# Kernel tuning notes

Measured on AMD Instinct MI355X. Metric: run time of the kernel, lower is better.

Reference implementation:

```python
import jax, jax.numpy as jnp
import numpy as np


def setup_inputs() -> dict:
    key = jax.random.key(0)
    ks = jax.random.split(key, 12)
    B, T, S, H, I = 32, 32, 400, 1024, 1024
    s = 0.02  # weight init scale
    return {
        "input_": jax.random.normal(ks[0], (B, T, I), jnp.float32),
        "h0": jax.random.normal(ks[1], (B, H), jnp.float32),
        "c0": jax.random.normal(ks[2], (B, H), jnp.float32),
        "h_attn0": jax.random.normal(ks[3], (B, H), jnp.float32),
        "encoder_hy": jax.random.normal(ks[4], (S, B, H), jnp.float32),
        "past_attn": jax.random.uniform(ks[5], (B, S), jnp.float32),
        "W_ih": jax.random.normal(ks[6], (4 * H, I + H), jnp.float32) * s,
        "W_hh": jax.random.normal(ks[7], (4 * H, H), jnp.float32) * s,
        "b_ih": jnp.zeros((4 * H,), jnp.float32),
        "b_hh": jnp.zeros((4 * H,), jnp.float32),
        "W_attn": jax.random.normal(ks[8], (H, H), jnp.float32) * s,
        "W_out": jax.random.normal(ks[9], (H, 2 * H), jnp.float32) * s,
    }


def _decode(input_, h0, c0, h_attn0, encoder_hy, W_ih, W_hh, b_ih, b_hh, W_attn, W_out):
    # encoder_hy: [S, B, H] -> enhy: [B, S, H]
    enhy = jnp.transpose(encoder_hy, (1, 0, 2))
    # attn_in(enhy) is time-invariant (linear, fixed enhy): hoist out of the loop
    enhy_new = jnp.einsum("bsh,gh->bsg", enhy, W_attn)  # [B, S, H]
    xs = jnp.transpose(input_, (1, 0, 2))  # [T, B, I] (batch_first)

    def step(carry, x_k):
        h, c, h_attn = carry
        x = jnp.concatenate([x_k, h_attn], axis=1)  # [B, I+H]
        gates = x @ W_ih.T + b_ih + h @ W_hh.T + b_hh  # [B, 4H]
        i, f, g, o = jnp.split(gates, 4, axis=1)  # torch LSTMCell gate order
        i = jax.nn.sigmoid(i)
        f = jax.nn.sigmoid(f)
        g = jnp.tanh(g)
        o = jax.nn.sigmoid(o)
        c = f * c + i * g
        h = o * jnp.tanh(c)
        # luong_general: attn = bmm(attn_in(enhy), dehy)
        attn = jax.nn.softmax(jnp.einsum("bsh,bh->bs", enhy_new, h), axis=1)
        ctx = jnp.einsum("bs,bsh->bh", attn, enhy)
        h_attn = jnp.tanh(jnp.concatenate([ctx, h], axis=1) @ W_out.T)
        return (h, c, h_attn), (h_attn, attn)

    (h, c, h_attn), (outs, attns) = jax.lax.scan(step, (h0, c0, h_attn0), xs)
    output = jnp.transpose(outs, (1, 0, 2))  # [B, T, H] (batch_first)
    return output, h, c, h_attn, attns  # attns: [T, B, S]


def reference(input_, h0, c0, h_attn0, encoder_hy, past_attn,
              W_ih, W_hh, b_ih, b_hh, W_attn, W_out):
    output, h, c, h_attn, out_attn = _decode(
        input_, h0, c0, h_attn0, encoder_hy, W_ih, W_hh, b_ih, b_hh, W_attn, W_out)
    # coverage='none': past_attn passes through unchanged; loss_cv stays 0.0
    return output, h, c, h_attn, out_attn, past_attn, jnp.float32(0.0)
```

## Files before the change

kernel.cpp:

```cpp
#include <hip/hip_runtime.h>
#include <hip/hip_bf16.h>

using u16 = unsigned short;
typedef __attribute__((ext_vector_type(8))) short bf16x8;
typedef __attribute__((ext_vector_type(4))) float f32x4;
typedef __attribute__((ext_vector_type(4))) u16 u16x4;


__device__ __forceinline__ float bf2f(u16 u){ union{unsigned int i; float f;} v; v.i = ((unsigned int)u)<<16; return v.f; }
__device__ __forceinline__ u16 f2bf(float f){ __hip_bfloat16 h = __float2bfloat16(f); return *reinterpret_cast<u16*>(&h); }
struct HL { u16 h, l; };
__device__ __forceinline__ HL split1(float f){
  HL r; r.h = f2bf(f); r.l = f2bf(f - bf2f(r.h)); return r;
}
__device__ __forceinline__ f32x4 mfma16(bf16x8 a, bf16x8 b, f32x4 c){ return __builtin_amdgcn_mfma_f32_16x16x32_bf16(a,b,c,0,0,0); }


__global__ __launch_bounds__(256) void cast_wih_k(const float* __restrict__ Wih,
    u16* __restrict__ Wxh, u16* __restrict__ Wxl, u16* __restrict__ Wrh, u16* __restrict__ Wrl){
  int v = blockIdx.x*256 + threadIdx.x;
  if (v >= (4096*2048)/4) return;
  int flat = v*4; int j = flat >> 11; int k = flat & 2047;
  float4 f = *(const float4*)(Wih + flat);
  HL s0 = split1(f.x), s1 = split1(f.y), s2 = split1(f.z), s3 = split1(f.w);
  u16x4 h, l;
  h[0]=s0.h; h[1]=s1.h; h[2]=s2.h; h[3]=s3.h;
  l[0]=s0.l; l[1]=s1.l; l[2]=s2.l; l[3]=s3.l;
  if (k < 1024){
    *(u16x4*)(Wxh + (size_t)j*1024 + k) = h;
    *(u16x4*)(Wxl + (size_t)j*1024 + k) = l;
  } else {
    *(u16x4*)(Wrh + (size_t)j*2048 + (k-1024)) = h;
    *(u16x4*)(Wrl + (size_t)j*2048 + (k-1024)) = l;
  }
}

__global__ __launch_bounds__(256) void cast_whh_k(const float* __restrict__ Whh,
    u16* __restrict__ Wrh, u16* __restrict__ Wrl){
  int v = blockIdx.x*256 + threadIdx.x;
  if (v >= (4096*1024)/4) return;
  int flat = v*4; int j = flat >> 10; int k = flat & 1023;
  float4 f = *(const float4*)(Whh + flat);
  HL s0 = split1(f.x), s1 = split1(f.y), s2 = split1(f.z), s3 = split1(f.w);
  u16x4 h, l;
  h[0]=s0.h; h[1]=s1.h; h[2]=s2.h; h[3]=s3.h;
  l[0]=s0.l; l[1]=s1.l; l[2]=s2.l; l[3]=s3.l;
  *(u16x4*)(Wrh + (size_t)j*2048 + 1024 + k) = h;
  *(u16x4*)(Wrl + (size_t)j*2048 + 1024 + k) = l;
}

__global__ __launch_bounds__(256) void cast_split_k(const float* __restrict__ src,
    u16* __restrict__ dh, u16* __restrict__ dl, int n4){
  int v = blockIdx.x*256 + threadIdx.x;
  if (v >= n4) return;
  float4 f = *(const float4*)(src + (size_t)v*4);
  HL s0 = split1(f.x), s1 = split1(f.y), s2 = split1(f.z), s3 = split1(f.w);
  u16x4 h, l;
  h[0]=s0.h; h[1]=s1.h; h[2]=s2.h; h[3]=s3.h;
  l[0]=s0.l; l[1]=s1.l; l[2]=s2.l; l[3]=s3.l;
  *(u16x4*)(dh + (size_t)v*4) = h;
  *(u16x4*)(dl + (size_t)v*4) = l;
}

__global__ __launch_bounds__(256) void cast_x_k(const float* __restrict__ inp,
    u16* __restrict__ Xh, u16* __restrict__ Xl){
  int v = blockIdx.x*256 + threadIdx.x;
  if (v >= (1024*1024)/4) return;
  int flat = v*4; int m = flat >> 10; int k = flat & 1023;
  int t = m >> 5, b = m & 31;
  float4 f = *(const float4*)(inp + ((size_t)(b*32 + t) << 10) + k);
  HL s0 = split1(f.x), s1 = split1(f.y), s2 = split1(f.z), s3 = split1(f.w);
  u16x4 h, l;
  h[0]=s0.h; h[1]=s1.h; h[2]=s2.h; h[3]=s3.h;
  l[0]=s0.l; l[1]=s1.l; l[2]=s2.l; l[3]=s3.l;
  *(u16x4*)(Xh + flat) = h;
  *(u16x4*)(Xl + flat) = l;
}

__global__ __launch_bounds__(256) void watsplit_k(const float* __restrict__ Wattn,
    u16* __restrict__ Wth, u16* __restrict__ Wtl){
  __shared__ float t[32][33];
  int gx = blockIdx.x, cx = blockIdx.y;
  int ty = threadIdx.x >> 5, tx = threadIdx.x & 31;
  #pragma unroll
  for (int i=0;i<4;++i){
    int g = gx*32 + ty + i*8;
    t[ty+i*8][tx] = Wattn[(size_t)g*1024 + cx*32 + tx];
  }
  __syncthreads();
  #pragma unroll
  for (int i=0;i<4;++i){
    int c = cx*32 + ty + i*8;
    HL s = split1(t[tx][ty+i*8]);
    Wth[(size_t)c*1024 + gx*32 + tx] = s.h;
    Wtl[(size_t)c*1024 + gx*32 + tx] = s.l;
  }
}

__global__ __launch_bounds__(256) void cast_encb_k(const float* __restrict__ enc,
    u16* __restrict__ encb){
  int v = blockIdx.x*256 + threadIdx.x;
  if (v >= (400*32*1024)/8) return;
  size_t flat = (size_t)v*8;
  int c = flat & 1023; int rem = flat >> 10;
  int b = rem & 31, s = rem >> 5;
  float4 f0 = *(const float4*)(enc + flat);
  float4 f1 = *(const float4*)(enc + flat + 4);
  u16x4 h0, h1;
  h0[0]=f2bf(f0.x); h0[1]=f2bf(f0.y); h0[2]=f2bf(f0.z); h0[3]=f2bf(f0.w);
  h1[0]=f2bf(f1.x); h1[1]=f2bf(f1.y); h1[2]=f2bf(f1.z); h1[3]=f2bf(f1.w);
  u16* dst = encb + ((size_t)b*400 + s)*1024 + c;
  *(u16x4*)dst = h0;
  *(u16x4*)(dst+4) = h1;
}

__global__ __launch_bounds__(256) void init_misc_k(const float* __restrict__ h0, const float* __restrict__ c0,
    const float* __restrict__ ha0, const float* __restrict__ past,
    u16* __restrict__ Zh0, u16* __restrict__ Zl0, float* __restrict__ cbuf,
    float* __restrict__ out_past, float* __restrict__ out_loss){
  int idx = blockIdx.x*256 + threadIdx.x;
  if (idx < 65536){
    int b = idx >> 11, col = idx & 2047;
    float v = (col < 1024) ? ha0[b*1024 + col] : h0[b*1024 + col - 1024];
    HL s = split1(v);
    Zh0[idx] = s.h; Zl0[idx] = s.l;
  } else if (idx < 65536 + 32768){
    int i = idx - 65536; cbuf[i] = c0[i];
  } else if (idx < 65536 + 32768 + 12800){
    int i = idx - 98304; out_past[i] = past[i];
  } else if (idx == 65536 + 32768 + 12800){
    out_loss[0] = 0.f;
  }
}

__global__ __launch_bounds__(256) void gemm128_bias_k(
    const u16* __restrict__ Ah, const u16* __restrict__ Al,
    const u16* __restrict__ Bh, const u16* __restrict__ Bl, float* __restrict__ C,
    const float* __restrict__ bias0, const float* __restrict__ bias1, int M, int N, int K)
{
  __shared__ __align__(16) u16 Ash[4096], Asl[4096], Bsh[4096], Bsl[4096];
  const int tid = threadIdx.x;
  const int lane = tid & 63, w = tid >> 6;
  const int wm = w >> 1, wn = w & 1;
  const int m0 = blockIdx.y * 128, n0 = blockIdx.x * 128;
  const int r = lane & 15, q = lane >> 4;

  f32x4 acc[4][4];
  #pragma unroll
  for (int i=0;i<4;i++)
    #pragma unroll
    for (int j=0;j<4;j++) acc[i][j] = (f32x4){0.f,0.f,0.f,0.f};

  const int NT = K >> 5;
  const int srow = tid >> 2;
  const int skp  = (tid & 3) * 8;
  bf16x8 rah0, rah1, ral0, ral1, rbh0, rbh1, rbl0, rbl1;

  {
    size_t ao = (size_t)(m0 + srow) * K + skp;
    size_t bo = (size_t)(n0 + srow) * K + skp;
    rah0 = *(const bf16x8*)(Ah + ao);  rah1 = *(const bf16x8*)(Ah + ao + (size_t)64*K);
    ral0 = *(const bf16x8*)(Al + ao);  ral1 = *(const bf16x8*)(Al + ao + (size_t)64*K);
    rbh0 = *(const bf16x8*)(Bh + bo);  rbh1 = *(const bf16x8*)(Bh + bo + (size_t)64*K);
    rbl0 = *(const bf16x8*)(Bl + bo);  rbl1 = *(const bf16x8*)(Bl + bo + (size_t)64*K);
  }

  for (int kt = 0; kt < NT; ++kt){
    __syncthreads();
    *(bf16x8*)(Ash + tid*8)        = rah0;
    *(bf16x8*)(Ash + 2048 + tid*8) = rah1;
    *(bf16x8*)(Asl + tid*8)        = ral0;
    *(bf16x8*)(Asl + 2048 + tid*8) = ral1;
    *(bf16x8*)(Bsh + tid*8)        = rbh0;
    *(bf16x8*)(Bsh + 2048 + tid*8) = rbh1;
    *(bf16x8*)(Bsl + tid*8)        = rbl0;
    *(bf16x8*)(Bsl + 2048 + tid*8) = rbl1;
    __syncthreads();
    if (kt + 1 < NT){
      size_t ao = (size_t)(m0 + srow) * K + (kt+1)*32 + skp;
      size_t bo = (size_t)(n0 + srow) * K + (kt+1)*32 + skp;
      rah0 = *(const bf16x8*)(Ah + ao);  rah1 = *(const bf16x8*)(Ah + ao + (size_t)64*K);
      ral0 = *(const bf16x8*)(Al + ao);  ral1 = *(const bf16x8*)(Al + ao + (size_t)64*K);
      rbh0 = *(const bf16x8*)(Bh + bo);  rbh1 = *(const bf16x8*)(Bh + bo + (size_t)64*K);
      rbl0 = *(const bf16x8*)(Bl + bo);  rbl1 = *(const bf16x8*)(Bl + bo + (size_t)64*K);
    }
    bf16x8 afh[4], afl[4], bfh[4], bfl[4];
    #pragma unroll
    for (int mf=0; mf<4; ++mf){
      int off = (wm*64 + mf*16 + r)*32 + q*8;
      afh[mf] = *(const bf16x8*)(Ash + off);
      afl[mf] = *(const bf16x8*)(Asl + off);
    }
    #pragma unroll
    for (int nf=0; nf<4; ++nf){
      int off = (wn*64 + nf*16 + r)*32 + q*8;
      bfh[nf] = *(const bf16x8*)(Bsh + off);
      bfl[nf] = *(const bf16x8*)(Bsl + off);
    }
    #pragma unroll
    for (int mf=0; mf<4; ++mf)
      #pragma unroll
      for (int nf=0; nf<4; ++nf){
        acc[mf][nf] = mfma16(afh[mf], bfh[nf], acc[mf][nf]);
        acc[mf][nf] = mfma16(afh[mf], bfl[nf], acc[mf][nf]);
        acc[mf][nf] = mfma16(afl[mf], bfh[nf], acc[mf][nf]);
      }
  }

  #pragma unroll
  for (int mf=0; mf<4; ++mf)
    #pragma unroll
    for (int nf=0; nf<4; ++nf)
      #pragma unroll
      for (int rr=0; rr<4; ++rr){
        int row = m0 + wm*64 + mf*16 + q*4 + rr;
        int col = n0 + wn*64 + nf*16 + r;
        C[(size_t)row*N + col] = acc[mf][nf][rr] + bias0[col] + bias1[col];
      }
}


__global__ __launch_bounds__(512) void rec_partial_k(
    const u16* __restrict__ Zh, const u16* __restrict__ Zl,
    const u16* __restrict__ Wh, const u16* __restrict__ Wl,
    float* __restrict__ recp)
{
  __shared__ float red[8][512];
  const int tid = threadIdx.x, lane = tid & 63, w = tid >> 6;
  const int g = w & 3, kh = w >> 2;
  const int jc = blockIdx.x & 63, kq = blockIdx.x >> 6;
  const int r = lane & 15, q = lane >> 4;
  const int k0 = kq*256 + kh*128;

  f32x4 acc0 = (f32x4){0,0,0,0}, acc1 = (f32x4){0,0,0,0};
  const size_t aoff = (size_t)r*2048 + k0 + q*8;
  const size_t boff = (size_t)(g*1024 + jc*16 + r)*2048 + k0 + q*8;
  #pragma unroll
  for (int kt = 0; kt < 4; ++kt){
    bf16x8 a0h = *(const bf16x8*)(Zh + aoff + kt*32);
    bf16x8 a0l = *(const bf16x8*)(Zl + aoff + kt*32);
    bf16x8 a1h = *(const bf16x8*)(Zh + aoff + (size_t)16*2048 + kt*32);
    bf16x8 a1l = *(const bf16x8*)(Zl + aoff + (size_t)16*2048 + kt*32);
    bf16x8 bh  = *(const bf16x8*)(Wh + boff + kt*32);
    bf16x8 bl  = *(const bf16x8*)(Wl + boff + kt*32);
    acc0 = mfma16(a0h, bh, acc0);
    acc0 = mfma16(a0h, bl, acc0);
    acc0 = mfma16(a0l, bh, acc0);
    acc1 = mfma16(a1h, bh, acc1);
    acc1 = mfma16(a1h, bl, acc1);
    acc1 = mfma16(a1l, bh, acc1);
  }
  #pragma unroll
  for (int rr=0; rr<4; ++rr){
    red[w][(q*4+rr)*16 + r]      = acc0[rr];
    red[w][(16 + q*4+rr)*16 + r] = acc1[rr];
  }
  __syncthreads();
  {
    int b = tid >> 4, jj = tid & 15;
    #pragma unroll
    for (int g2=0; g2<4; ++g2){
      float v = red[g2][tid] + red[g2+4][tid];
      recp[((size_t)kq*32 + b)*4096 + g2*1024 + jc*16 + jj] = v;
    }
  }
}

__global__ __launch_bounds__(256) void cell_k(
    const float* __restrict__ recp, const float* __restrict__ gX,
    float* __restrict__ cbuf, u16* __restrict__ Znh, u16* __restrict__ Znl,
    u16* __restrict__ Zoh, u16* __restrict__ Zol,
    float* __restrict__ out_h, float* __restrict__ out_c, int last)
{
  int idx = blockIdx.x*256 + threadIdx.x;
  int b = idx >> 10, j = idx & 1023;
  float gs[4];
  #pragma unroll
  for (int g=0; g<4; ++g){
    float v = gX[(size_t)b*4096 + g*1024 + j];
    #pragma unroll
    for (int kq=0; kq<8; ++kq) v += recp[((size_t)kq*32 + b)*4096 + g*1024 + j];
    gs[g] = v;
  }
  float iv = 1.f/(1.f + expf(-gs[0]));
  float fv = 1.f/(1.f + expf(-gs[1]));
  float gv = tanhf(gs[2]);
  float ov = 1.f/(1.f + expf(-gs[3]));
  float cn = fv * cbuf[idx] + iv*gv;
  cbuf[idx] = cn;
  float h = ov * tanhf(cn);
  HL s = split1(h);
  size_t zi = (size_t)b*2048 + 1024 + j;
  Znh[zi] = s.h; Znl[zi] = s.l;
  Zoh[zi] = s.h; Zol[zi] = s.l;
  if (last){ out_h[idx] = h; out_c[idx] = cn; }
}

__global__ __launch_bounds__(512) void u_mfma_k(
    const u16* __restrict__ Zoh, const u16* __restrict__ Zol,
    const u16* __restrict__ Wth, const u16* __restrict__ Wtl,
    float* __restrict__ ubuf)
{
  __shared__ float red[8][512];
  const int tid = threadIdx.x, lane = tid & 63, w = tid >> 6;
  const int cc = blockIdx.x;
  const int r = lane & 15, q = lane >> 4;
  f32x4 acc0 = (f32x4){0,0,0,0}, acc1 = (f32x4){0,0,0,0};
  const size_t aoff = (size_t)r*2048 + 1024 + w*128 + q*8;
  const size_t boff = (size_t)(cc*16 + r)*1024 + w*128 + q*8;
  #pragma unroll
  for (int kt=0; kt<4; ++kt){
    bf16x8 a0h = *(const bf16x8*)(Zoh + aoff + kt*32);
    bf16x8 a0l = *(const bf16x8*)(Zol + aoff + kt*32);
    bf16x8 a1h = *(const bf16x8*)(Zoh + aoff + (size_t)16*2048 + kt*32);
    bf16x8 a1l = *(const bf16x8*)(Zol + aoff + (size_t)16*2048 + kt*32);
    bf16x8 bh  = *(const bf16x8*)(Wth + boff + kt*32);
    bf16x8 bl  = *(const bf16x8*)(Wtl + boff + kt*32);
    acc0 = mfma16(a0h, bh, acc0);
    acc0 = mfma16(a0h, bl, acc0);
    acc0 = mfma16(a0l, bh, acc0);
    acc1 = mfma16(a1h, bh, acc1);
    acc1 = mfma16(a1h, bl, acc1);
    acc1 = mfma16(a1l, bh, acc1);
  }
  #pragma unroll
  for (int rr=0; rr<4; ++rr){
    red[w][(q*4+rr)*16 + r]      = acc0[rr];
    red[w][(16 + q*4+rr)*16 + r] = acc1[rr];
  }
  __syncthreads();
  {
    int b = tid >> 4, jj = tid & 15;
    float v = 0.f;
    #pragma unroll
    for (int w2=0; w2<8; ++w2) v += red[w2][tid];
    ubuf[(size_t)b*1024 + cc*16 + jj] = v;
  }
}

__global__ __launch_bounds__(512) void flash_bf16_k(const u16* __restrict__ encb,
    const float* __restrict__ ubuf, float* __restrict__ scbuf,
    float* __restrict__ ctxp, float* __restrict__ mlbuf)
{
  __shared__ float wacc[8][1024];
  __shared__ float wml[16];
  const int tid = threadIdx.x, lane = tid & 63, w = tid >> 6;
  const int b = blockIdx.x >> 4, sc16 = blockIdx.x & 15;
  const int s0 = sc16 * 25;

  const float* up = ubuf + (size_t)b*1024 + lane*16;
  float uu[16];
  #pragma unroll
  for (int i=0;i<4;i++){ float4 t4 = *(const float4*)(up + i*4); uu[4*i]=t4.x; uu[4*i+1]=t4.y; uu[4*i+2]=t4.z; uu[4*i+3]=t4.w; }

  float m = -1e30f, l = 0.f;
  float acc[16];
  #pragma unroll
  for (int i=0;i<16;i++) acc[i] = 0.f;

  for (int s = s0 + w; s < s0 + 25; s += 8){
    const u16* ep = encb + ((size_t)b*400 + s)*1024 + lane*16;
    bf16x8 e0 = *(const bf16x8*)ep;
    bf16x8 e1 = *(const bf16x8*)(ep + 8);
    float er[16];
    #pragma unroll
    for (int i=0;i<8;i++){ er[i] = bf2f((u16)e0[i]); er[8+i] = bf2f((u16)e1[i]); }
    float sc = 0.f;
    #pragma unroll
    for (int i=0;i<16;i++) sc = fmaf(er[i], uu[i], sc);
    #pragma unroll
    for (int off=32; off; off>>=1) sc += __shfl_xor(sc, off);
    if (lane == 0) scbuf[(size_t)b*400 + s] = sc;
    if (sc > m){
      float f = expf(m - sc);
      l *= f;
      #pragma unroll
      for (int i=0;i<16;i++) acc[i] *= f;
      m = sc;
    }
    float wgt = expf(sc - m);
    l += wgt;
    #pragma unroll
    for (int i=0;i<16;i++) acc[i] = fmaf(wgt, er[i], acc[i]);
  }

  #pragma unroll
  for (int i=0;i<16;i++) wacc[w][lane*16+i] = acc[i];
  if (lane == 0){ wml[w*2] = m; wml[w*2+1] = l; }
  __syncthreads();

  float M = wml[0];
  #pragma unroll
  for (int i=1;i<8;i++) M = fmaxf(M, wml[i*2]);
  float c0v = 0.f, c1v = 0.f;
  #pragma unroll
  for (int i=0;i<8;i++){
    float f = expf(wml[i*2] - M);
    c0v = fmaf(wacc[i][tid],       f, c0v);
    c1v = fmaf(wacc[i][tid + 512], f, c1v);
  }
  size_t co = ((size_t)b*16 + sc16)*1024;
  ctxp[co + tid]       = c0v;
  ctxp[co + tid + 512] = c1v;
  if (tid == 0){
    float L = 0.f;
    #pragma unroll
    for (int i=0;i<8;i++) L += wml[i*2+1] * expf(wml[i*2] - M);
    mlbuf[((size_t)b*16 + sc16)*2]     = M;
    mlbuf[((size_t)b*16 + sc16)*2 + 1] = L;
  }
}

__global__ __launch_bounds__(512) void flash_f32_k(const float* __restrict__ enc,
    const float* __restrict__ ubuf, float* __restrict__ scbuf,
    float* __restrict__ ctxp, float* __restrict__ mlbuf)
{
  __shared__ float wacc[8][1024];
  __shared__ float wml[16];
  const int tid = threadIdx.x, lane = tid & 63, w = tid >> 6;
  const int b = blockIdx.x >> 4, sc16 = blockIdx.x & 15;
  const int s0 = sc16 * 25;

  const float* up = ubuf + (size_t)b*1024 + lane*16;
  float uu[16];
  #pragma unroll
  for (int i=0;i<4;i++){ float4 t4 = *(const float4*)(up + i*4); uu[4*i]=t4.x; uu[4*i+1]=t4.y; uu[4*i+2]=t4.z; uu[4*i+3]=t4.w; }

  float m = -1e30f, l = 0.f;
  float acc[16];
  #pragma unroll
  for (int i=0;i<16;i++) acc[i] = 0.f;

  for (int s = s0 + w; s < s0 + 25; s += 8){
    const float* ep = enc + ((size_t)s*32 + b)*1024 + lane*16;
    float er[16];
    #pragma unroll
    for (int i=0;i<4;i++){ float4 e4 = *(const float4*)(ep + i*4); er[4*i]=e4.x; er[4*i+1]=e4.y; er[4*i+2]=e4.z; er[4*i+3]=e4.w; }
    float sc = 0.f;
    #pragma unroll
    for (int i=0;i<16;i++) sc = fmaf(er[i], uu[i], sc);
    #pragma unroll
    for (int off=32; off; off>>=1) sc += __shfl_xor(sc, off);
    if (lane == 0) scbuf[(size_t)b*400 + s] = sc;
    if (sc > m){
      float f = expf(m - sc);
      l *= f;
      #pragma unroll
      for (int i=0;i<16;i++) acc[i] *= f;
      m = sc;
    }
    float wgt = expf(sc - m);
    l += wgt;
    #pragma unroll
    for (int i=0;i<16;i++) acc[i] = fmaf(wgt, er[i], acc[i]);
  }

  #pragma unroll
  for (int i=0;i<16;i++) wacc[w][lane*16+i] = acc[i];
  if (lane == 0){ wml[w*2] = m; wml[w*2+1] = l; }
  __syncthreads();

  float M = wml[0];
  #pragma unroll
  for (int i=1;i<8;i++) M = fmaxf(M, wml[i*2]);
  float c0v = 0.f, c1v = 0.f;
  #pragma unroll
  for (int i=0;i<8;i++){
    float f = expf(wml[i*2] - M);
    c0v = fmaf(wacc[i][tid],       f, c0v);
    c1v = fmaf(wacc[i][tid + 512], f, c1v);
  }
  size_t co = ((size_t)b*16 + sc16)*1024;
  ctxp[co + tid]       = c0v;
  ctxp[co + tid + 512] = c1v;
  if (tid == 0){
    float L = 0.f;
    #pragma unroll
    for (int i=0;i<8;i++) L += wml[i*2+1] * expf(wml[i*2] - M);
    mlbuf[((size_t)b*16 + sc16)*2]     = M;
    mlbuf[((size_t)b*16 + sc16)*2 + 1] = L;
  }
}

__global__ __launch_bounds__(256) void combine_k(const float* __restrict__ scbuf,
    const float* __restrict__ ctxp, const float* __restrict__ mlbuf,
    u16* __restrict__ Zoh, u16* __restrict__ Zol, float* __restrict__ attn_out)
{
  const int b = blockIdx.x >> 3, cc = blockIdx.x & 7;
  const int tid = threadIdx.x;
  float M = -1e30f;
  #pragma unroll
  for (int i=0;i<16;i++) M = fmaxf(M, mlbuf[((size_t)b*16 + i)*2]);
  float L = 0.f;
  #pragma unroll
  for (int i=0;i<16;i++) L += mlbuf[((size_t)b*16 + i)*2 + 1] * expf(mlbuf[((size_t)b*16 + i)*2] - M);
  float invL = 1.f / L;
  if (tid < 128){
    int col = cc*128 + tid;
    float v = 0.f;
    #pragma unroll
    for (int i=0;i<16;i++)
      v = fmaf(ctxp[((size_t)b*16 + i)*1024 + col], expf(mlbuf[((size_t)b*16 + i)*2] - M), v);
    HL s = split1(v * invL);
    size_t zi = (size_t)b*2048 + col;
    Zoh[zi] = s.h; Zol[zi] = s.l;
  } else if (tid < 128 + 50){
    int s = cc*50 + (tid - 128);
    attn_out[(size_t)b*400 + s] = expf(scbuf[(size_t)b*400 + s] - M) * invL;
  }
}

__global__ __launch_bounds__(512) void outg_partial_k(
    const u16* __restrict__ Zoh, const u16* __restrict__ Zol,
    const u16* __restrict__ Woh, const u16* __restrict__ Wol,
    float* __restrict__ outp)
{
  __shared__ float red[8][512];
  const int tid = threadIdx.x, lane = tid & 63, w = tid >> 6;
  const int jc = blockIdx.x & 63, kq = blockIdx.x >> 6;
  const int r = lane & 15, q = lane >> 4;
  const int k0 = kq*256 + w*32;
  f32x4 acc0 = (f32x4){0,0,0,0}, acc1 = (f32x4){0,0,0,0};
  const size_t aoff = (size_t)r*2048 + k0 + q*8;
  const size_t boff = (size_t)(jc*16 + r)*2048 + k0 + q*8;
  {
    bf16x8 a0h = *(const bf16x8*)(Zoh + aoff);
    bf16x8 a0l = *(const bf16x8*)(Zol + aoff);
    bf16x8 a1h = *(const bf16x8*)(Zoh + aoff + (size_t)16*2048);
    bf16x8 a1l = *(const bf16x8*)(Zol + aoff + (size_t)16*2048);
    bf16x8 bh  = *(const bf16x8*)(Woh + boff);
    bf16x8 bl  = *(const bf16x8*)(Wol + boff);
    acc0 = mfma16(a0h, bh, acc0);
    acc0 = mfma16(a0h, bl, acc0);
    acc0 = mfma16(a0l, bh, acc0);
    acc1 = mfma16(a1h, bh, acc1);
    acc1 = mfma16(a1h, bl, acc1);
    acc1 = mfma16(a1l, bh, acc1);
  }
  #pragma unroll
  for (int rr=0; rr<4; ++rr){
    red[w][(q*4+rr)*16 + r]      = acc0[rr];
    red[w][(16 + q*4+rr)*16 + r] = acc1[rr];
  }
  __syncthreads();
  {
    int b = tid >> 4, jj = tid & 15;
    float v = 0.f;
    #pragma unroll
    for (int w2=0; w2<8; ++w2) v += red[w2][tid];
    outp[((size_t)kq*32 + b)*1024 + jc*16 + jj] = v;
  }
}

__global__ __launch_bounds__(256) void outred_k(const float* __restrict__ outp,
    float* __restrict__ out_outp, u16* __restrict__ Znh, u16* __restrict__ Znl,
    float* __restrict__ out_hattn, int last)
{
  int idx = blockIdx.x*256 + threadIdx.x;
  int b = idx >> 10, uc = idx & 1023;
  float z = 0.f;
  #pragma unroll
  for (int kq=0; kq<8; ++kq) z += outp[((size_t)kq*32 + b)*1024 + uc];
  float ha = tanhf(z);
  out_outp[(size_t)b*32768 + uc] = ha;
  HL s = split1(ha);
  Znh[(size_t)b*2048 + uc] = s.h;
  Znl[(size_t)b*2048 + uc] = s.l;
  if (last) out_hattn[(size_t)b*1024 + uc] = ha;
}


extern "C" void kernel_launch(void* const* d_in, const int* in_sizes, int n_in,
                              void* d_out, int out_size, void* d_ws, size_t ws_size,
                              hipStream_t stream)
{
  const float* input_ = (const float*)d_in[0];
  const float* h0     = (const float*)d_in[1];
  const float* c0     = (const float*)d_in[2];
  const float* ha0    = (const float*)d_in[3];
  const float* enc    = (const float*)d_in[4];
  const float* past   = (const float*)d_in[5];
  const float* W_ih   = (const float*)d_in[6];
  const float* W_hh   = (const float*)d_in[7];
  const float* b_ih   = (const float*)d_in[8];
  const float* b_hh   = (const float*)d_in[9];
  const float* W_attn = (const float*)d_in[10];
  const float* W_out  = (const float*)d_in[11];
  float* out = (float*)d_out;

  const size_t OUT_OUTPUT = 0;
  const size_t OUT_H      = 1048576;
  const size_t OUT_C      = 1081344;
  const size_t OUT_HATTN  = 1114112;
  const size_t OUT_ATTN   = 1146880;
  const size_t OUT_PAST   = 1556480;
  const size_t OUT_LOSS   = 1569280;

  const size_t OFF_WRH   = 0;
  const size_t OFF_WRL   = 16777216;
  const size_t OFF_WXH   = 33554432;
  const size_t OFF_WXL   = 41943040;
  const size_t OFF_WOH   = 50331648;
  const size_t OFF_WOL   = 54525952;
  const size_t OFF_XBH   = 58720256;
  const size_t OFF_XBL   = 60817408;
  const size_t OFF_GATEX = 62914560;
  const size_t OFF_ZBH   = 79691776;
  const size_t OFF_ZBL   = 79953920;
  const size_t OFF_ZOH   = 80216064;
  const size_t OFF_ZOL   = 80347136;
  const size_t OFF_CBUF  = 80478208;
  const size_t OFF_UBUF  = 80609280;
  const size_t OFF_SC    = 80740352;
  const size_t OFF_PAD   = 80842752;
  const size_t WS_NEED   = 82939904;
  if (ws_size < WS_NEED) return;

  const size_t OFF_ENCB  = WS_NEED;
  const size_t WS_BIG    = WS_NEED + 26214400;
  const bool use_bf16enc = (ws_size >= WS_BIG);

  const size_t OFF_CTXP  = OFF_WXH;
  const size_t OFF_ML    = OFF_WXH + 2097152;
  const size_t OFF_OUTP  = OFF_WXH + 3145728;
  const size_t OFF_RECP  = OFF_WXL;

  char* ws = (char*)d_ws;
  u16*   Wrh   = (u16*)(ws + OFF_WRH);
  u16*   Wrl   = (u16*)(ws + OFF_WRL);
  u16*   Wxh   = (u16*)(ws + OFF_WXH);
  u16*   Wxl   = (u16*)(ws + OFF_WXL);
  u16*   Woh   = (u16*)(ws + OFF_WOH);
  u16*   Wol   = (u16*)(ws + OFF_WOL);
  u16*   Xbh   = (u16*)(ws + OFF_XBH);
  u16*   Xbl   = (u16*)(ws + OFF_XBL);
  u16*   Wth   = (u16*)(ws + OFF_XBH);
  u16*   Wtl   = (u16*)(ws + OFF_XBL);
  float* gateX = (float*)(ws + OFF_GATEX);
  u16*   Zbh   = (u16*)(ws + OFF_ZBH);
  u16*   Zbl   = (u16*)(ws + OFF_ZBL);
  u16*   Zoh   = (u16*)(ws + OFF_ZOH);
  u16*   Zol   = (u16*)(ws + OFF_ZOL);
  float* cbuf  = (float*)(ws + OFF_CBUF);
  float* ubuf  = (float*)(ws + OFF_UBUF);
  float* sc    = (float*)(ws + OFF_SC);
  float* ctxp  = (float*)(ws + OFF_CTXP);
  float* mlbuf = (float*)(ws + OFF_ML);
  float* outp  = (float*)(ws + OFF_OUTP);
  float* recp  = (float*)(ws + OFF_RECP);
  u16*   encb  = (u16*)(ws + OFF_ENCB);

  cast_wih_k <<<8192, 256, 0, stream>>>(W_ih, Wxh, Wxl, Wrh, Wrl);
  cast_whh_k <<<4096, 256, 0, stream>>>(W_hh, Wrh, Wrl);
  cast_split_k<<<2048, 256, 0, stream>>>(W_out, Woh, Wol, (1024*2048)/4);
  cast_x_k   <<<1024, 256, 0, stream>>>(input_, Xbh, Xbl);
  init_misc_k<<<435, 256, 0, stream>>>(h0, c0, ha0, past, Zbh, Zbl, cbuf, out + OUT_PAST, out + OUT_LOSS);
  if (use_bf16enc)
    cast_encb_k<<<6400, 256, 0, stream>>>(enc, encb);

  gemm128_bias_k<<<dim3(32, 8), 256, 0, stream>>>(Xbh, Xbl, Wxh, Wxl, gateX, b_ih, b_hh, 1024, 4096, 1024);
  watsplit_k<<<dim3(32, 32), 256, 0, stream>>>(W_attn, Wth, Wtl);

  for (int t = 0; t < 32; ++t){
    int p = t & 1;
    u16* Zih = Zbh + (size_t)p * 65536;
    u16* Zil = Zbl + (size_t)p * 65536;
    u16* Znh = Zbh + (size_t)(1-p) * 65536;
    u16* Znl = Zbl + (size_t)(1-p) * 65536;
    int last = (t == 31);
    rec_partial_k<<<512, 512, 0, stream>>>(Zih, Zil, Wrh, Wrl, recp);
    cell_k<<<128, 256, 0, stream>>>(recp, gateX + (size_t)t*131072, cbuf,
        Znh, Znl, Zoh, Zol, out + OUT_H, out + OUT_C, last);
    u_mfma_k<<<64, 512, 0, stream>>>(Zoh, Zol, Wth, Wtl, ubuf);
    if (use_bf16enc)
      flash_bf16_k<<<512, 512, 0, stream>>>(encb, ubuf, sc, ctxp, mlbuf);
    else
      flash_f32_k<<<512, 512, 0, stream>>>(enc, ubuf, sc, ctxp, mlbuf);
    combine_k<<<256, 256, 0, stream>>>(sc, ctxp, mlbuf, Zoh, Zol,
        out + OUT_ATTN + (size_t)t*12800);
    outg_partial_k<<<512, 512, 0, stream>>>(Zoh, Zol, Woh, Wol, outp);
    outred_k<<<128, 256, 0, stream>>>(outp, out + OUT_OUTPUT + (size_t)t*1024,
        Znh, Znl, out + OUT_HATTN, last);
  }
}
```

Measured before the change: 1.437 ms.

## Fuse recurrent GEMM with LSTM cell and output GEMM with its reduction

The recurrent gate GEMM now gives each block all four gates for four hidden units over the full K range, so the partial sums are reduced in shared memory and the LSTM cell update runs in the same kernel. The output projection likewise reduces over full K inside one block and applies tanh directly. This drops two kernel launches per timestep and the global partial-sum buffers. In exchange there are fewer blocks (256 and 128) with longer K loops per wave, which may lower parallelism and latency hiding.

```diff
diff --git a/kernel.cpp b/kernel.cpp
--- a/kernel.cpp
+++ b/kernel.cpp
@@ -220,23 +220,26 @@
 }
 
 
-__global__ __launch_bounds__(512) void rec_partial_k(
+__global__ __launch_bounds__(512) void rec_cell_k(
     const u16* __restrict__ Zh, const u16* __restrict__ Zl,
     const u16* __restrict__ Wh, const u16* __restrict__ Wl,
-    float* __restrict__ recp)
+    const float* __restrict__ gX, float* __restrict__ cbuf,
+    u16* __restrict__ Znh, u16* __restrict__ Znl,
+    u16* __restrict__ Zoh, u16* __restrict__ Zol,
+    float* __restrict__ out_h, float* __restrict__ out_c, int last)
 {
   __shared__ float red[8][512];
+  __shared__ float gsum[512];
   const int tid = threadIdx.x, lane = tid & 63, w = tid >> 6;
-  const int g = w & 3, kh = w >> 2;
-  const int jc = blockIdx.x & 63, kq = blockIdx.x >> 6;
+  const int j4 = blockIdx.x;
   const int r = lane & 15, q = lane >> 4;
-  const int k0 = kq*256 + kh*128;
+  const int k0 = w*256;
 
   f32x4 acc0 = (f32x4){0,0,0,0}, acc1 = (f32x4){0,0,0,0};
   const size_t aoff = (size_t)r*2048 + k0 + q*8;
-  const size_t boff = (size_t)(g*1024 + jc*16 + r)*2048 + k0 + q*8;
-  #pragma unroll
-  for (int kt = 0; kt < 4; ++kt){
+  const size_t boff = (size_t)((r>>2)*1024 + j4*4 + (r&3))*2048 + k0 + q*8;
+  #pragma unroll
+  for (int kt = 0; kt < 8; ++kt){
     bf16x8 a0h = *(const bf16x8*)(Zh + aoff + kt*32);
     bf16x8 a0l = *(const bf16x8*)(Zl + aoff + kt*32);
     bf16x8 a1h = *(const bf16x8*)(Zh + aoff + (size_t)16*2048 + kt*32);
@@ -252,48 +255,38 @@
   }
   #pragma unroll
   for (int rr=0; rr<4; ++rr){
-    red[w][(q*4+rr)*16 + r]      = acc0[rr];
-    red[w][(16 + q*4+rr)*16 + r] = acc1[rr];
+    red[w][(q*4+rr)*16 + r]        = acc0[rr];
+    red[w][256 + (q*4+rr)*16 + r]  = acc1[rr];
   }
   __syncthreads();
   {
-    int b = tid >> 4, jj = tid & 15;
-    #pragma unroll
-    for (int g2=0; g2<4; ++g2){
-      float v = red[g2][tid] + red[g2+4][tid];
-      recp[((size_t)kq*32 + b)*4096 + g2*1024 + jc*16 + jj] = v;
-    }
-  }
-}
-
-__global__ __launch_bounds__(256) void cell_k(
-    const float* __restrict__ recp, const float* __restrict__ gX,
-    float* __restrict__ cbuf, u16* __restrict__ Znh, u16* __restrict__ Znl,
-    u16* __restrict__ Zoh, u16* __restrict__ Zol,
-    float* __restrict__ out_h, float* __restrict__ out_c, int last)
-{
-  int idx = blockIdx.x*256 + threadIdx.x;
-  int b = idx >> 10, j = idx & 1023;
-  float gs[4];
-  #pragma unroll
-  for (int g=0; g<4; ++g){
-    float v = gX[(size_t)b*4096 + g*1024 + j];
-    #pragma unroll
-    for (int kq=0; kq<8; ++kq) v += recp[((size_t)kq*32 + b)*4096 + g*1024 + j];
-    gs[g] = v;
-  }
-  float iv = 1.f/(1.f + expf(-gs[0]));
-  float fv = 1.f/(1.f + expf(-gs[1]));
-  float gv = tanhf(gs[2]);
-  float ov = 1.f/(1.f + expf(-gs[3]));
-  float cn = fv * cbuf[idx] + iv*gv;
-  cbuf[idx] = cn;
-  float h = ov * tanhf(cn);
-  HL s = split1(h);
-  size_t zi = (size_t)b*2048 + 1024 + j;
-  Znh[zi] = s.h; Znl[zi] = s.l;
-  Zoh[zi] = s.h; Zol[zi] = s.l;
-  if (last){ out_h[idx] = h; out_c[idx] = cn; }
+    float v = 0.f;
+    #pragma unroll
+    for (int w2=0; w2<8; ++w2) v += red[w2][tid];
+    gsum[tid] = v;
+  }
+  __syncthreads();
+  if (tid < 128){
+    int b = tid >> 2, c = tid & 3;
+    int j = j4*4 + c;
+    float gs[4];
+    #pragma unroll
+    for (int g=0; g<4; ++g)
+      gs[g] = gsum[b*16 + g*4 + c] + gX[(size_t)b*4096 + g*1024 + j];
+    int idx = b*1024 + j;
+    float iv = 1.f/(1.f + expf(-gs[0]));
+    float fv = 1.f/(1.f + expf(-gs[1]));
+    float gv = tanhf(gs[2]);
+    float ov = 1.f/(1.f + expf(-gs[3]));
+    float cn = fv * cbuf[idx] + iv*gv;
+    cbuf[idx] = cn;
+    float h = ov * tanhf(cn);
+    HL s = split1(h);
+    size_t zi = (size_t)b*2048 + 1024 + j;
+    Znh[zi] = s.h; Znl[zi] = s.l;
+    Zoh[zi] = s.h; Zol[zi] = s.l;
+    if (last){ out_h[idx] = h; out_c[idx] = cn; }
+  }
 }
 
 __global__ __launch_bounds__(512) void u_mfma_k(
@@ -510,63 +503,48 @@
   }
 }
 
-__global__ __launch_bounds__(512) void outg_partial_k(
+__global__ __launch_bounds__(512) void outg_fused_k(
     const u16* __restrict__ Zoh, const u16* __restrict__ Zol,
     const u16* __restrict__ Woh, const u16* __restrict__ Wol,
-    float* __restrict__ outp)
-{
-  __shared__ float red[8][512];
+    float* __restrict__ out_outp , u16* __restrict__ Znh, u16* __restrict__ Znl,
+    float* __restrict__ out_hattn, int last)
+{
+  __shared__ float red[8][256];
   const int tid = threadIdx.x, lane = tid & 63, w = tid >> 6;
-  const int jc = blockIdx.x & 63, kq = blockIdx.x >> 6;
+  const int ub = blockIdx.x & 63, bh = blockIdx.x >> 6;
   const int r = lane & 15, q = lane >> 4;
-  const int k0 = kq*256 + w*32;
-  f32x4 acc0 = (f32x4){0,0,0,0}, acc1 = (f32x4){0,0,0,0};
-  const size_t aoff = (size_t)r*2048 + k0 + q*8;
-  const size_t boff = (size_t)(jc*16 + r)*2048 + k0 + q*8;
-  {
-    bf16x8 a0h = *(const bf16x8*)(Zoh + aoff);
-    bf16x8 a0l = *(const bf16x8*)(Zol + aoff);
-    bf16x8 a1h = *(const bf16x8*)(Zoh + aoff + (size_t)16*2048);
-    bf16x8 a1l = *(const bf16x8*)(Zol + aoff + (size_t)16*2048);
-    bf16x8 bh  = *(const bf16x8*)(Woh + boff);
-    bf16x8 bl  = *(const bf16x8*)(Wol + boff);
-    acc0 = mfma16(a0h, bh, acc0);
-    acc0 = mfma16(a0h, bl, acc0);
-    acc0 = mfma16(a0l, bh, acc0);
-    acc1 = mfma16(a1h, bh, acc1);
-    acc1 = mfma16(a1h, bl, acc1);
-    acc1 = mfma16(a1l, bh, acc1);
-  }
-  #pragma unroll
-  for (int rr=0; rr<4; ++rr){
-    red[w][(q*4+rr)*16 + r]      = acc0[rr];
-    red[w][(16 + q*4+rr)*16 + r] = acc1[rr];
-  }
+  const int k0 = w*256;
+  f32x4 acc0 = (f32x4){0,0,0,0};
+  const size_t aoff = (size_t)(bh*16 + r)*2048 + k0 + q*8;
+  const size_t boff = (size_t)(ub*16 + r)*2048 + k0 + q*8;
+  #pragma unroll
+  for (int kt=0; kt<8; ++kt){
+    bf16x8 ah = *(const bf16x8*)(Zoh + aoff + kt*32);
+    bf16x8 al = *(const bf16x8*)(Zol + aoff + kt*32);
+    bf16x8 bh_ = *(const bf16x8*)(Woh + boff + kt*32);
+    bf16x8 bl_ = *(const bf16x8*)(Wol + boff + kt*32);
+    acc0 = mfma16(ah, bh_, acc0);
+    acc0 = mfma16(ah, bl_, acc0);
+    acc0 = mfma16(al, bh_, acc0);
+  }
+  #pragma unroll
+  for (int rr=0; rr<4; ++rr)
+    red[w][(q*4+rr)*16 + r] = acc0[rr];
   __syncthreads();
-  {
-    int b = tid >> 4, jj = tid & 15;
-    float v = 0.f;
-    #pragma unroll
-    for (int w2=0; w2<8; ++w2) v += red[w2][tid];
-    outp[((size_t)kq*32 + b)*1024 + jc*16 + jj] = v;
-  }
-}
-
-__global__ __launch_bounds__(256) void outred_k(const float* __restrict__ outp,
-    float* __restrict__ out_outp, u16* __restrict__ Znh, u16* __restrict__ Znl,
-    float* __restrict__ out_hattn, int last)
-{
-  int idx = blockIdx.x*256 + threadIdx.x;
-  int b = idx >> 10, uc = idx & 1023;
-  float z = 0.f;
-  #pragma unroll
-  for (int kq=0; kq<8; ++kq) z += outp[((size_t)kq*32 + b)*1024 + uc];
-  float ha = tanhf(z);
-  out_outp[(size_t)b*32768 + uc] = ha;
-  HL s = split1(ha);
-  Znh[(size_t)b*2048 + uc] = s.h;
-  Znl[(size_t)b*2048 + uc] = s.l;
-  if (last) out_hattn[(size_t)b*1024 + uc] = ha;
+  if (tid < 256){
+    int bloc = tid >> 4, jj = tid & 15;
+    float z = 0.f;
+    #pragma unroll
+    for (int w2=0; w2<8; ++w2) z += red[w2][tid];
+    int b = bh*16 + bloc;
+    int u = ub*16 + jj;
+    float ha = tanhf(z);
+    out_outp[(size_t)b*32768 + u] = ha;
+    HL s = split1(ha);
+    Znh[(size_t)b*2048 + u] = s.h;
+    Znl[(size_t)b*2048 + u] = s.l;
+    if (last) out_hattn[(size_t)b*1024 + u] = ha;
+  }
 }
 
 
@@ -612,7 +590,6 @@
   const size_t OFF_CBUF  = 80478208;
   const size_t OFF_UBUF  = 80609280;
   const size_t OFF_SC    = 80740352;
-  const size_t OFF_PAD   = 80842752;
   const size_t WS_NEED   = 82939904;
   if (ws_size < WS_NEED) return;
 
@@ -622,8 +599,6 @@
 
   const size_t OFF_CTXP  = OFF_WXH;
   const size_t OFF_ML    = OFF_WXH + 2097152;
-  const size_t OFF_OUTP  = OFF_WXH + 3145728;
-  const size_t OFF_RECP  = OFF_WXL;
 
   char* ws = (char*)d_ws;
   u16*   Wrh   = (u16*)(ws + OFF_WRH);
@@ -646,8 +621,6 @@
   float* sc    = (float*)(ws + OFF_SC);
   float* ctxp  = (float*)(ws + OFF_CTXP);
   float* mlbuf = (float*)(ws + OFF_ML);
-  float* outp  = (float*)(ws + OFF_OUTP);
-  float* recp  = (float*)(ws + OFF_RECP);
   u16*   encb  = (u16*)(ws + OFF_ENCB);
 
   cast_wih_k <<<8192, 256, 0, stream>>>(W_ih, Wxh, Wxl, Wrh, Wrl);
@@ -668,9 +641,9 @@
     u16* Znh = Zbh + (size_t)(1-p) * 65536;
     u16* Znl = Zbl + (size_t)(1-p) * 65536;
     int last = (t == 31);
-    rec_partial_k<<<512, 512, 0, stream>>>(Zih, Zil, Wrh, Wrl, recp);
-    cell_k<<<128, 256, 0, stream>>>(recp, gateX + (size_t)t*131072, cbuf,
-        Znh, Znl, Zoh, Zol, out + OUT_H, out + OUT_C, last);
+    rec_cell_k<<<256, 512, 0, stream>>>(Zih, Zil, Wrh, Wrl,
+        gateX + (size_t)t*131072, cbuf, Znh, Znl, Zoh, Zol,
+        out + OUT_H, out + OUT_C, last);
     u_mfma_k<<<64, 512, 0, stream>>>(Zoh, Zol, Wth, Wtl, ubuf);
     if (use_bf16enc)
       flash_bf16_k<<<512, 512, 0, stream>>>(encb, ubuf, sc, ctxp, mlbuf);
@@ -678,8 +651,7 @@
       flash_f32_k<<<512, 512, 0, stream>>>(enc, ubuf, sc, ctxp, mlbuf);
     combine_k<<<256, 256, 0, stream>>>(sc, ctxp, mlbuf, Zoh, Zol,
         out + OUT_ATTN + (size_t)t*12800);
-    outg_partial_k<<<512, 512, 0, stream>>>(Zoh, Zol, Woh, Wol, outp);
-    outred_k<<<128, 256, 0, stream>>>(outp, out + OUT_OUTPUT + (size_t)t*1024,
-        Znh, Znl, out + OUT_HATTN, last);
-  }
-}
+    outg_fused_k<<<128, 512, 0, stream>>>(Zoh, Zol, Woh, Wol,
+        out + OUT_OUTPUT + (size_t)t*1024, Znh, Znl, out + OUT_HATTN, last);
+  }
+}
```

Result: faster. 1.400 ms (-2.6%).
